# Kernel optimization log

Measured on AMD Instinct MI355X. Metric: run time of the kernel, lower is better.

Reference implementation:

```python
import jax, jax.numpy as jnp
import numpy as np

D_MODEL = 2048
N_HEADS = 32
N_KV = 8
HEAD_DIM = D_MODEL // N_HEADS  # 64
D_FF = 8192
ROPE_BASE = 10000.0
EPS = 1e-5
B, S = 2, 2048


def setup_inputs() -> dict:
    key = jax.random.key(0)
    ks = jax.random.split(key, 8)
    s = 0.02
    qkv_out = (N_HEADS + 2 * N_KV) * HEAD_DIM
    return {
        "x": jax.random.normal(ks[0], (B, S, D_MODEL), jnp.float32),
        "w_norm1": jnp.ones((D_MODEL,), jnp.float32),
        "w_qkv": jax.random.normal(ks[1], (D_MODEL, qkv_out), jnp.float32) * s,
        "w_out": jax.random.normal(ks[2], (D_MODEL, D_MODEL), jnp.float32) * s,
        "w_norm2": jnp.ones((D_MODEL,), jnp.float32),
        "w_gate": jax.random.normal(ks[3], (D_MODEL, D_FF), jnp.float32) * s,
        "w_up": jax.random.normal(ks[4], (D_MODEL, D_FF), jnp.float32) * s,
        "w_down": jax.random.normal(ks[5], (D_FF, D_MODEL), jnp.float32) * s,
    }


def _rmsnorm(x, w):
    var = jnp.mean(x * x, axis=-1, keepdims=True)
    return x * jax.lax.rsqrt(var + EPS) * w


def _rope(x, cos, sin):
    # x: [b, s, h, d]; cos/sin: [s, d/2]; non-interleaved (NeoX half split)
    half = x.shape[-1] // 2
    x1, x2 = x[..., :half], x[..., half:]
    c = cos[None, :, None, :]
    sn = sin[None, :, None, :]
    return jnp.concatenate([x1 * c - x2 * sn, x1 * sn + x2 * c], axis=-1)


def _forward(x, w_norm1, w_qkv, w_out, w_norm2, w_gate, w_up, w_down):
    b, s, d = x.shape
    # --- attention block ---
    h = _rmsnorm(x, w_norm1)
    qkv = h @ w_qkv  # [b, s, (H + 2*KV) * hd]
    q = qkv[..., : N_HEADS * HEAD_DIM].reshape(b, s, N_HEADS, HEAD_DIM)
    kv = qkv[..., N_HEADS * HEAD_DIM:].reshape(b, s, 2, N_KV, HEAD_DIM)
    k, v = kv[:, :, 0], kv[:, :, 1]

    inv_freq = 1.0 / (ROPE_BASE ** (jnp.arange(0, HEAD_DIM, 2, dtype=jnp.float32) / HEAD_DIM))
    t = jnp.arange(s, dtype=jnp.float32)
    freqs = t[:, None] * inv_freq[None, :]  # [s, hd/2]
    cos, sin = jnp.cos(freqs), jnp.sin(freqs)
    q = _rope(q, cos, sin)
    k = _rope(k, cos, sin)

    # GQA: repeat_interleave kv heads to match q heads
    g = N_HEADS // N_KV
    k = jnp.repeat(k, g, axis=2)  # [b, s, H, hd]
    v = jnp.repeat(v, g, axis=2)

    scale = 1.0 / np.sqrt(HEAD_DIM)
    scores = jnp.einsum("bqhd,bkhd->bhqk", q, k) * scale
    causal = jnp.tril(jnp.ones((s, s), bool))
    scores = jnp.where(causal[None, None], scores, jnp.finfo(scores.dtype).min)
    attn = jax.nn.softmax(scores, axis=-1)
    ctx = jnp.einsum("bhqk,bkhd->bqhd", attn, v).reshape(b, s, N_HEADS * HEAD_DIM)
    x = x + ctx @ w_out

    # --- MLP block (SwiGLU) ---
    h2 = _rmsnorm(x, w_norm2)
    mlp = (jax.nn.silu(h2 @ w_gate) * (h2 @ w_up)) @ w_down
    return x + mlp


def reference(x, w_norm1, w_qkv, w_out, w_norm2, w_gate, w_up, w_down):
    return _forward(x, w_norm1, w_qkv, w_out, w_norm2, w_gate, w_up, w_down)
```

## Files before the change

### kernel.cpp

```cpp
#include <hip/hip_runtime.h>
#include <stdint.h>

#define D_MODEL 2048
#define S_LEN   2048
#define NTOK    4096
#define QKV_N   3072
#define DFF     8192

typedef float  f32x4   __attribute__((ext_vector_type(4)));
typedef float  f32x16  __attribute__((ext_vector_type(16)));
typedef __bf16 bf16x8  __attribute__((ext_vector_type(8)));
typedef unsigned short u16;
typedef unsigned short u16x8 __attribute__((ext_vector_type(8)));

__device__ __forceinline__ float b2f(u16 u){ union{float f; uint32_t i;} v; v.i = ((uint32_t)u) << 16; return v.f; }
__device__ __forceinline__ u16 f2b(float f){
  union{float f; uint32_t i;} v; v.f = f;
  uint32_t r = v.i + 0x7FFFu + ((v.i >> 16) & 1u);
  return (u16)(r >> 16);
}

__device__ __forceinline__ void gload_lds16(const void* gsrc, void* ldst){
  __builtin_amdgcn_global_load_lds(
      (const __attribute__((address_space(1))) void*)gsrc,
      (__attribute__((address_space(3))) void*)ldst,
      16, 0, 0);
}

__global__ __launch_bounds__(256) void wconv_kernel(const float* __restrict__ W, u16* __restrict__ WT,
                                                    int Nfull, int Kt, int Nt, int k0g, int n0g)
{
  __shared__ float tile[64][65];
  const int nTn = Nt >> 6;
  const int tk = blockIdx.x / nTn, tn = blockIdx.x % nTn;
  const int k0 = tk << 6, n0 = tn << 6;
  const int t  = threadIdx.x;
  const int c4 = (t & 15) << 2;
  const int r  = t >> 4;
#pragma unroll
  for (int i = 0; i < 4; ++i) {
    float4 v = *reinterpret_cast<const float4*>(&W[(size_t)(k0g + k0 + r + i*16) * Nfull + n0g + n0 + c4]);
    tile[r + i*16][c4+0] = v.x; tile[r + i*16][c4+1] = v.y;
    tile[r + i*16][c4+2] = v.z; tile[r + i*16][c4+3] = v.w;
  }
  __syncthreads();
#pragma unroll
  for (int i = 0; i < 4; ++i) {
    int n = r + i*16;
    ushort4 ov;
    ov.x = f2b(tile[c4+0][n]); ov.y = f2b(tile[c4+1][n]);
    ov.z = f2b(tile[c4+2][n]); ov.w = f2b(tile[c4+3][n]);
    *reinterpret_cast<ushort4*>(&WT[(size_t)(n0 + n) * Kt + k0 + c4]) = ov;
  }
}

__global__ void sincos_kernel(float* __restrict__ ct, float* __restrict__ st)
{
  int idx = blockIdx.x * 256 + threadIdx.x;
  if (idx >= S_LEN * 32) return;
  int p = idx >> 5, i = idx & 31;
  double freq = pow(10000.0, -((double)(2*i)) / 64.0);
  double ang  = (double)p * freq;
  ct[idx] = (float)cos(ang);
  st[idx] = (float)sin(ang);
}

template<bool BF16IN>
__global__ __launch_bounds__(256) void rmsnorm_kernel(const void* __restrict__ xin, const float* __restrict__ w, u16* __restrict__ out)
{
  const int row = blockIdx.x;
  const int t = threadIdx.x;
  float v[8];
  if (BF16IN) {
    const u16* xr = ((const u16*)xin) + (size_t)row * D_MODEL;
    u16x8 a = *reinterpret_cast<const u16x8*>(&xr[t*8]);
#pragma unroll
    for (int j = 0; j < 8; ++j) v[j] = b2f(a[j]);
  } else {
    const float* xr = ((const float*)xin) + (size_t)row * D_MODEL;
    float4 a = *reinterpret_cast<const float4*>(&xr[t*8]);
    float4 c = *reinterpret_cast<const float4*>(&xr[t*8+4]);
    v[0]=a.x; v[1]=a.y; v[2]=a.z; v[3]=a.w; v[4]=c.x; v[5]=c.y; v[6]=c.z; v[7]=c.w;
  }
  float ss = 0.f;
#pragma unroll
  for (int j = 0; j < 8; ++j) ss += v[j]*v[j];
#pragma unroll
  for (int d = 1; d < 64; d <<= 1) ss += __shfl_xor(ss, d);
  __shared__ float red[4];
  if ((t & 63) == 0) red[t >> 6] = ss;
  __syncthreads();
  ss = red[0] + red[1] + red[2] + red[3];
  const float sc = rsqrtf(ss * (1.0f / (float)D_MODEL) + 1e-5f);
  float4 w0 = *reinterpret_cast<const float4*>(&w[t*8]);
  float4 w1 = *reinterpret_cast<const float4*>(&w[t*8+4]);
  u16x8 o;
  o[0]=f2b(v[0]*sc*w0.x); o[1]=f2b(v[1]*sc*w0.y); o[2]=f2b(v[2]*sc*w0.z); o[3]=f2b(v[3]*sc*w0.w);
  o[4]=f2b(v[4]*sc*w1.x); o[5]=f2b(v[5]*sc*w1.y); o[6]=f2b(v[6]*sc*w1.z); o[7]=f2b(v[7]*sc*w1.w);
  *reinterpret_cast<u16x8*>(&out[(size_t)row * D_MODEL + t*8]) = o;
}

template<int EPI>
__global__ __launch_bounds__(512, 2) void gemm8p_kernel(
    const u16* __restrict__ A, const u16* __restrict__ BT,
    int K, int lda, int ldb, int ldc, int n_off,
    float* Cf, u16* Cb,
    const float* __restrict__ resf, const u16* __restrict__ resb, const u16* other)
{
  __shared__ u16 lds[65536];
  const int tid = threadIdx.x;
  const int w = tid >> 6, lane = tid & 63;
  const int g = lane >> 4, lr = lane & 15;
  const int wm = w >> 2, wn = w & 3;
  const int bn = blockIdx.x, bm = blockIdx.y;
  const int NT = K >> 6;
  const int NI = NT >> 1;

  const int srow = tid >> 3;
  const int sg   = (tid & 7) ^ (srow & 7);
  const u16* Asrc = A  + (size_t)(bm * 256) * lda;
  const u16* Bsrc = BT + (size_t)(bn * 256) * ldb;

  const int agc0 = ((0 + g) ^ (lr & 7)) * 8;
  const int agc1 = ((4 + g) ^ (lr & 7)) * 8;

  f32x4 acc[8][4];
#pragma unroll
  for (int i = 0; i < 8; ++i)
#pragma unroll
    for (int j = 0; j < 4; ++j) acc[i][j] = (f32x4){0.f, 0.f, 0.f, 0.f};
  bf16x8 af[4][2], bf0[2][2], bf1[2][2];

#define STAGE_H(isB, h, b, T) do {                                           \
    int tc = ((T) < NT) ? (T) : (NT - 1);                                    \
    const u16* sb = (isB) ? Bsrc : Asrc;                                     \
    const int  sld = (isB) ? ldb : lda;                                      \
    const u16* s0 = sb + (size_t)((h)*128 + srow) * sld + tc*64 + sg*8;      \
    u16* dst = &lds[(b)*32768 + (isB)*16384 + (h)*8192 + tid*8];             \
    gload_lds16(s0, dst);                                                    \
    gload_lds16(s0 + (size_t)64 * sld, dst + 4096);                          \
  } while (0)

#define LOADA(mih, b) { _Pragma("unroll") for (int q = 0; q < 4; ++q) {      \
    const u16* rp = &lds[(b)*32768 + (wm*128 + (mih)*64 + q*16 + lr) * 64];  \
    af[q][0] = *(const bf16x8*)(rp + agc0);                                  \
    af[q][1] = *(const bf16x8*)(rp + agc1); } }

#define LOADB(dst, nih, b) { _Pragma("unroll") for (int nq = 0; nq < 2; ++nq) { \
    const u16* rp = &lds[(b)*32768 + 16384 + (wn*64 + (nih)*32 + nq*16 + lr) * 64]; \
    dst[nq][0] = *(const bf16x8*)(rp + agc0);                                \
    dst[nq][1] = *(const bf16x8*)(rp + agc1); } }

#define MM(mih, nih, BF) {                                                   \
    __builtin_amdgcn_s_setprio(1);                                           \
    _Pragma("unroll") for (int kk = 0; kk < 2; ++kk)                         \
      _Pragma("unroll") for (int q = 0; q < 4; ++q)                          \
        _Pragma("unroll") for (int nq = 0; nq < 2; ++nq)                     \
          acc[(mih)*4+q][(nih)*2+nq] = __builtin_amdgcn_mfma_f32_16x16x32_bf16( \
              af[q][kk], BF[nq][kk], acc[(mih)*4+q][(nih)*2+nq], 0, 0, 0);   \
    __builtin_amdgcn_s_setprio(0); }

#define SYNC_MID  __builtin_amdgcn_s_barrier();                              \
                  asm volatile("s_waitcnt lgkmcnt(0)" ::: "memory");         \
                  __builtin_amdgcn_sched_barrier(0);
#define PHEND     __builtin_amdgcn_s_barrier();
#define PHEND_VM  asm volatile("s_waitcnt vmcnt(4)" ::: "memory");           \
                  __builtin_amdgcn_s_barrier();

  STAGE_H(0, 0, 0, 0); STAGE_H(0, 1, 0, 0);
  STAGE_H(1, 0, 0, 0); STAGE_H(1, 1, 0, 0);
  STAGE_H(1, 0, 1, 1); STAGE_H(1, 1, 1, 1);
  asm volatile("s_waitcnt vmcnt(4)" ::: "memory");
  __builtin_amdgcn_s_barrier();

  for (int i = 0; i < NI; ++i) {
    const int t0 = 2 * i;
    LOADA(0, 0); LOADB(bf0, 0, 0);
    STAGE_H(0, 0, 1, t0 + 1);
    SYNC_MID; MM(0, 0, bf0); PHEND;
    LOADB(bf1, 1, 0);
    STAGE_H(0, 1, 1, t0 + 1);
    SYNC_MID; MM(0, 1, bf1); PHEND;
    LOADA(1, 0);
    STAGE_H(1, 0, 0, t0 + 2);
    SYNC_MID; MM(1, 1, bf1); PHEND;
    STAGE_H(1, 1, 0, t0 + 2);
    SYNC_MID; MM(1, 0, bf0); PHEND_VM;
    LOADA(0, 1); LOADB(bf0, 0, 1);
    STAGE_H(0, 0, 0, t0 + 2);
    SYNC_MID; MM(0, 0, bf0); PHEND;
    LOADB(bf1, 1, 1);
    STAGE_H(0, 1, 0, t0 + 2);
    SYNC_MID; MM(0, 1, bf1); PHEND;
    LOADA(1, 1);
    STAGE_H(1, 0, 1, t0 + 3);
    SYNC_MID; MM(1, 1, bf1); PHEND;
    STAGE_H(1, 1, 1, t0 + 3);
    SYNC_MID; MM(1, 0, bf0); PHEND_VM;
  }
#undef STAGE_H
#undef LOADA
#undef LOADB
#undef MM
#undef SYNC_MID
#undef PHEND
#undef PHEND_VM

#pragma unroll
  for (int mi = 0; mi < 8; ++mi) {
    const int rowOff = (mi >> 2) * 64 + (mi & 3) * 16;
#pragma unroll
    for (int ni = 0; ni < 4; ++ni) {
      const int colOff = (ni >> 1) * 32 + (ni & 1) * 16;
#pragma unroll
      for (int j = 0; j < 4; ++j) {
        int row = bm*256 + wm*128 + rowOff + g*4 + j;
        int col = n_off + bn*256 + wn*64 + colOff + lr;
        size_t idx = (size_t)row * ldc + col;
        float v = acc[mi][ni][j];
        if (EPI == 2)      Cb[idx] = f2b(v / (1.0f + __expf(-v)));
        else if (EPI == 3) Cb[idx] = f2b(v * b2f(other[idx]));
        else if (EPI == 4) Cb[idx] = f2b(v);
        else if (EPI == 5) Cf[idx] += v;
        else if (EPI == 6) Cb[idx] = f2b(v + resf[idx]);
        else if (EPI == 7) Cf[idx] = v + b2f(resb[idx]);
      }
    }
  }
}

__global__ __launch_bounds__(256) void rope_kernel(
    const u16* __restrict__ qkv, const float* __restrict__ ct, const float* __restrict__ st,
    u16* __restrict__ Q, u16* __restrict__ Kt, u16* __restrict__ VT)
{
  const int tok = blockIdx.x;
  const int b = tok >> 11, s = tok & (S_LEN - 1);
  const int w = threadIdx.x >> 6, lane = threadIdx.x & 63;
  const size_t base = (size_t)tok * QKV_N;
  for (int slot = w; slot < 48; slot += 4) {
    int col = (slot < 32) ? slot * 64 : (slot < 40 ? 2048 + (slot - 32) * 64 : 2560 + (slot - 40) * 64);
    float v = b2f(qkv[base + col + lane]);
    if (slot < 40) {
      int i = lane & 31;
      float c = ct[s * 32 + i], sn = st[s * 32 + i];
      float p = b2f(qkv[base + col + (lane ^ 32)]);
      v = (lane < 32) ? (v * c - p * sn) : (v * c + p * sn);
    }
    u16 ob = f2b(v);
    if (slot < 32)      Q [((size_t)(b * 32 + slot)      * S_LEN + s) * 64 + lane] = ob;
    else if (slot < 40) Kt[((size_t)(b * 8 + slot - 32)  * S_LEN + s) * 64 + lane] = ob;
    else                VT[((size_t)(b * 8 + slot - 40)  * 64 + lane) * S_LEN + s] = ob;
  }
}

#define ASCALE 0.1803368801111204f
__global__ __launch_bounds__(256, 3) void attn_kernel(
    const u16* __restrict__ Q, const u16* __restrict__ Kt,
    const u16* __restrict__ VT, u16* __restrict__ ctx)
{
  const int bh  = blockIdx.x;
  const int qb  = 15 - blockIdx.y;
  const int wid = threadIdx.x >> 6;
  const int lane = threadIdx.x & 63;
  const int b = bh >> 5, h = bh & 31;
  const int kvh = (b << 3) + (h >> 2);
  const int q0 = qb * 128 + wid * 32;
  const int cq = lane & 31;
  const int hi = lane >> 5;

  const u16* Qb = Q  + ((size_t)bh * S_LEN + q0) * 64;
  const u16* Kb = Kt + (size_t)kvh * S_LEN * 64;
  const u16* Vb = VT + (size_t)kvh * 64 * S_LEN;

  bf16x8 qf[4];
#pragma unroll
  for (int t = 0; t < 4; ++t)
    qf[t] = *reinterpret_cast<const bf16x8*>(&Qb[cq * 64 + t * 16 + hi * 8]);

  f32x16 o0 = {}, o1 = {};
  float m = -1e30f, l = 0.f;

  __shared__ float xch[4][32];

  const int nt = (q0 >> 5) + 1;
  for (int t = 0; t < nt; ++t) {
    const int k0 = t << 5;
    bf16x8 kf[4], vf[4];
#pragma unroll
    for (int tt = 0; tt < 4; ++tt)
      kf[tt] = *reinterpret_cast<const bf16x8*>(&Kb[(size_t)(k0 + cq) * 64 + tt * 16 + hi * 8]);
#pragma unroll
    for (int kh = 0; kh < 2; ++kh)
#pragma unroll
      for (int dh = 0; dh < 2; ++dh)
        vf[kh * 2 + dh] = *reinterpret_cast<const bf16x8*>(&Vb[(size_t)(dh * 32 + cq) * S_LEN + k0 + kh * 16 + hi * 8]);

    f32x16 sA = {}, sB = {};
    sA = __builtin_amdgcn_mfma_f32_32x32x16_bf16(kf[0], qf[0], sA, 0, 0, 0);
    sB = __builtin_amdgcn_mfma_f32_32x32x16_bf16(kf[1], qf[1], sB, 0, 0, 0);
    sA = __builtin_amdgcn_mfma_f32_32x32x16_bf16(kf[2], qf[2], sA, 0, 0, 0);
    sB = __builtin_amdgcn_mfma_f32_32x32x16_bf16(kf[3], qf[3], sB, 0, 0, 0);

    float p[16];
#pragma unroll
    for (int r = 0; r < 16; ++r) p[r] = (sA[r] + sB[r]) * ASCALE;
    if (t == nt - 1) {
#pragma unroll
      for (int r = 0; r < 16; ++r) {
        int kk = (r & 3) + 8 * (r >> 2) + 4 * hi;
        if (kk > cq) p[r] = -1e30f;
      }
    }
    float tmax = p[0];
#pragma unroll
    for (int r = 1; r < 16; ++r) tmax = fmaxf(tmax, p[r]);
    tmax = fmaxf(tmax, __shfl_xor(tmax, 32));

    if (!__all(tmax <= m + 8.0f)) {
      float mn = fmaxf(m, tmax);
      float corr = exp2f(m - mn);
      m = mn;
      l *= corr;
      if (hi == 0) xch[wid][cq] = corr;
      asm volatile("s_waitcnt lgkmcnt(0)" ::: "memory");
      __builtin_amdgcn_sched_barrier(0);
      float4 c0 = *reinterpret_cast<const float4*>(&xch[wid][4 * hi + 0]);
      float4 c1 = *reinterpret_cast<const float4*>(&xch[wid][4 * hi + 8]);
      float4 c2 = *reinterpret_cast<const float4*>(&xch[wid][4 * hi + 16]);
      float4 c3 = *reinterpret_cast<const float4*>(&xch[wid][4 * hi + 24]);
      float ca[16] = {c0.x,c0.y,c0.z,c0.w, c1.x,c1.y,c1.z,c1.w,
                      c2.x,c2.y,c2.z,c2.w, c3.x,c3.y,c3.z,c3.w};
#pragma unroll
      for (int r = 0; r < 16; ++r) { o0[r] *= ca[r]; o1[r] *= ca[r]; }
    }

    float ts = 0.f;
#pragma unroll
    for (int r = 0; r < 16; ++r) { p[r] = exp2f(p[r] - m); ts += p[r]; }
    ts += __shfl_xor(ts, 32);
    l += ts;

    uint32_t wds[8], pw[8];
#pragma unroll
    for (int j = 0; j < 8; ++j) {
      uint32_t wv;
      asm("v_cvt_pk_bf16_f32 %0, %1, %2" : "=v"(wv) : "v"(p[2*j]), "v"(p[2*j+1]));
      wds[j] = wv;
    }
#pragma unroll
    for (int j = 0; j < 8; ++j) pw[j] = __shfl_xor(wds[j], 32);
    union { uint32_t u[4]; bf16x8 v; } pa0, pa1;
    pa0.u[0] = hi ? pw[2]  : wds[0];
    pa0.u[1] = hi ? pw[3]  : wds[1];
    pa0.u[2] = hi ? wds[2] : pw[0];
    pa0.u[3] = hi ? wds[3] : pw[1];
    pa1.u[0] = hi ? pw[6]  : wds[4];
    pa1.u[1] = hi ? pw[7]  : wds[5];
    pa1.u[2] = hi ? wds[6] : pw[4];
    pa1.u[3] = hi ? wds[7] : pw[5];

    o0 = __builtin_amdgcn_mfma_f32_32x32x16_bf16(pa0.v, vf[0], o0, 0, 0, 0);
    o0 = __builtin_amdgcn_mfma_f32_32x32x16_bf16(pa1.v, vf[2], o0, 0, 0, 0);
    o1 = __builtin_amdgcn_mfma_f32_32x32x16_bf16(pa0.v, vf[1], o1, 0, 0, 0);
    o1 = __builtin_amdgcn_mfma_f32_32x32x16_bf16(pa1.v, vf[3], o1, 0, 0, 0);
  }

  float linv = 1.0f / l;
  if (hi == 0) xch[wid][cq] = linv;
  asm volatile("s_waitcnt lgkmcnt(0)" ::: "memory");
  __builtin_amdgcn_sched_barrier(0);
  float4 n0 = *reinterpret_cast<const float4*>(&xch[wid][4 * hi + 0]);
  float4 n1 = *reinterpret_cast<const float4*>(&xch[wid][4 * hi + 8]);
  float4 n2 = *reinterpret_cast<const float4*>(&xch[wid][4 * hi + 16]);
  float4 n3 = *reinterpret_cast<const float4*>(&xch[wid][4 * hi + 24]);
  float na[16] = {n0.x,n0.y,n0.z,n0.w, n1.x,n1.y,n1.z,n1.w,
                  n2.x,n2.y,n2.z,n2.w, n3.x,n3.y,n3.z,n3.w};
#pragma unroll
  for (int r = 0; r < 16; ++r) {
    int row = (r & 3) + 8 * (r >> 2) + 4 * hi;
    size_t base = (size_t)(b * S_LEN + q0 + row) * D_MODEL + h * 64;
    ctx[base + cq]      = f2b(o0[r] * na[r]);
    ctx[base + 32 + cq] = f2b(o1[r] * na[r]);
  }
}

extern "C" void kernel_launch(void* const* d_in, const int* in_sizes, int n_in,
                              void* d_out, int out_size, void* d_ws, size_t ws_size,
                              hipStream_t stream)
{
  const float* x     = (const float*)d_in[0];
  const float* wn1   = (const float*)d_in[1];
  const float* wqkv  = (const float*)d_in[2];
  const float* wout  = (const float*)d_in[3];
  const float* wn2   = (const float*)d_in[4];
  const float* wgate = (const float*)d_in[5];
  const float* wup   = (const float*)d_in[6];
  const float* wdown = (const float*)d_in[7];
  float* out = (float*)d_out;
  char* ws = (char*)d_ws;

  float* cosT = (float*)(ws + 0);
  float* sinT = (float*)(ws + 262144);
  u16*   wT   = (u16*)  (ws + 524288);
  u16*   hB   = (u16*)  (ws + 17301504);
  u16*   x1b  = (u16*)  (ws + 34078720);
  char*  S    = ws + 50855936;
  u16*   qkvB = (u16*)(S + 0);
  u16*   qB   = (u16*)(S + 25165824);
  u16*   kB   = (u16*)(S + 41943040);
  u16*   vtB  = (u16*)(S + 46137344);
  u16*   ctxB = (u16*)(S + 50331648);
  u16*   gsB  = (u16*)(S + 0);

  sincos_kernel<<<dim3(256), 256, 0, stream>>>(cosT, sinT);
  rmsnorm_kernel<false><<<dim3(NTOK), 256, 0, stream>>>(x, wn1, hB);

  wconv_kernel<<<dim3((2048/64)*(3072/64)), 256, 0, stream>>>(wqkv, wT, 3072, 2048, 3072, 0, 0);
  gemm8p_kernel<4><<<dim3(QKV_N/256, NTOK/256), 512, 0, stream>>>(hB, wT, 2048, 2048, 2048, 3072, 0, nullptr, qkvB, nullptr, nullptr, nullptr);
  rope_kernel<<<dim3(NTOK), 256, 0, stream>>>(qkvB, cosT, sinT, qB, kB, vtB);
  attn_kernel<<<dim3(64, 16), 256, 0, stream>>>(qB, kB, vtB, ctxB);

  wconv_kernel<<<dim3((2048/64)*(2048/64)), 256, 0, stream>>>(wout, wT, 2048, 2048, 2048, 0, 0);
  gemm8p_kernel<6><<<dim3(D_MODEL/256, NTOK/256), 512, 0, stream>>>(ctxB, wT, 2048, 2048, 2048, 2048, 0, nullptr, x1b, x, nullptr, nullptr);

  rmsnorm_kernel<true><<<dim3(NTOK), 256, 0, stream>>>(x1b, wn2, hB);

  for (int c = 0; c < 2; ++c) {
    wconv_kernel<<<dim3((2048/64)*(4096/64)), 256, 0, stream>>>(wgate, wT, 8192, 2048, 4096, 0, c*4096);
    gemm8p_kernel<2><<<dim3(4096/256, NTOK/256), 512, 0, stream>>>(hB, wT, 2048, 2048, 2048, 8192, c*4096, nullptr, gsB, nullptr, nullptr, nullptr);
  }
  for (int c = 0; c < 2; ++c) {
    wconv_kernel<<<dim3((2048/64)*(4096/64)), 256, 0, stream>>>(wup, wT, 8192, 2048, 4096, 0, c*4096);
    gemm8p_kernel<3><<<dim3(4096/256, NTOK/256), 512, 0, stream>>>(hB, wT, 2048, 2048, 2048, 8192, c*4096, nullptr, gsB, nullptr, nullptr, gsB);
  }
  wconv_kernel<<<dim3((4096/64)*(2048/64)), 256, 0, stream>>>(wdown, wT, 2048, 4096, 2048, 0, 0);
  gemm8p_kernel<7><<<dim3(D_MODEL/256, NTOK/256), 512, 0, stream>>>(gsB, wT, 4096, 8192, 4096, 2048, 0, out, nullptr, nullptr, x1b, nullptr);
  wconv_kernel<<<dim3((4096/64)*(2048/64)), 256, 0, stream>>>(wdown, wT, 2048, 4096, 2048, 4096, 0);
  gemm8p_kernel<5><<<dim3(D_MODEL/256, NTOK/256), 512, 0, stream>>>(gsB + 4096, wT, 4096, 8192, 4096, 2048, 0, out, nullptr, nullptr, nullptr, nullptr);
}
```

Before: 900.3 us.

## Add 128-row GEMM for small-N projections and split-K causal attention for late query blocks

Adds a 128x256-tile GEMM variant and uses it for the QKV, output and down projections. The smaller M tile doubles the block count on these narrow-N GEMMs so more of the GPU's compute units are busy. Attention now splits the key range of the eight longest causal query blocks across two workgroups, writing partial outputs with their max and sum statistics. A new combine kernel merges the two partials, which balances per-block work in exchange for an extra launch and more global traffic.

```diff
diff --git a/kernel.cpp b/kernel.cpp
--- a/kernel.cpp
+++ b/kernel.cpp
@@ -98,6 +98,18 @@
   o[0]=f2b(v[0]*sc*w0.x); o[1]=f2b(v[1]*sc*w0.y); o[2]=f2b(v[2]*sc*w0.z); o[3]=f2b(v[3]*sc*w0.w);
   o[4]=f2b(v[4]*sc*w1.x); o[5]=f2b(v[5]*sc*w1.y); o[6]=f2b(v[6]*sc*w1.z); o[7]=f2b(v[7]*sc*w1.w);
   *reinterpret_cast<u16x8*>(&out[(size_t)row * D_MODEL + t*8]) = o;
+}
+
+template<int EPI>
+__device__ __forceinline__ void epi_store(size_t idx, float v, float* Cf, u16* Cb,
+                                          const float* resf, const u16* resb, const u16* other)
+{
+  if (EPI == 2)      Cb[idx] = f2b(v / (1.0f + __expf(-v)));
+  else if (EPI == 3) Cb[idx] = f2b(v * b2f(other[idx]));
+  else if (EPI == 4) Cb[idx] = f2b(v);
+  else if (EPI == 5) Cf[idx] += v;
+  else if (EPI == 6) Cb[idx] = f2b(v + resf[idx]);
+  else if (EPI == 7) Cf[idx] = v + b2f(resb[idx]);
 }
 
 template<int EPI>
@@ -202,28 +214,141 @@
 #undef LOADA
 #undef LOADB
 #undef MM
+
+#pragma unroll
+  for (int mi = 0; mi < 8; ++mi) {
+    const int rowOff = (mi >> 2) * 64 + (mi & 3) * 16;
+#pragma unroll
+    for (int ni = 0; ni < 4; ++ni) {
+      const int colOff = (ni >> 1) * 32 + (ni & 1) * 16;
+#pragma unroll
+      for (int j = 0; j < 4; ++j) {
+        int row = bm*256 + wm*128 + rowOff + g*4 + j;
+        int col = n_off + bn*256 + wn*64 + colOff + lr;
+        epi_store<EPI>((size_t)row * ldc + col, acc[mi][ni][j], Cf, Cb, resf, resb, other);
+      }
+    }
+  }
+}
+
+template<int EPI>
+__global__ __launch_bounds__(512) void gemm128_kernel(
+    const u16* __restrict__ A, const u16* __restrict__ BT,
+    int K, int lda, int ldb, int ldc, int n_off,
+    float* Cf, u16* Cb,
+    const float* __restrict__ resf, const u16* __restrict__ resb, const u16* other)
+{
+  __shared__ u16 lds[49152];
+  const int tid = threadIdx.x;
+  const int w = tid >> 6, lane = tid & 63;
+  const int g = lane >> 4, lr = lane & 15;
+  const int wm = w >> 2, wn = w & 3;
+  const int bn = blockIdx.x, bm = blockIdx.y;
+  const int NT = K >> 6;
+  const int NI = NT >> 1;
+
+  const int srow = tid >> 3;
+  const int sg   = (tid & 7) ^ (srow & 7);
+  const u16* Asrc = A  + (size_t)(bm * 128) * lda;
+  const u16* Bsrc = BT + (size_t)(bn * 256) * ldb;
+
+  const int agc0 = ((0 + g) ^ (lr & 7)) * 8;
+  const int agc1 = ((4 + g) ^ (lr & 7)) * 8;
+
+  f32x4 acc[4][4];
+#pragma unroll
+  for (int i = 0; i < 4; ++i)
+#pragma unroll
+    for (int j = 0; j < 4; ++j) acc[i][j] = (f32x4){0.f, 0.f, 0.f, 0.f};
+  bf16x8 af[2][2], bf0[2][2], bf1[2][2];
+
+#define STAGE_A(b, T) do {                                                   \
+    int tc = ((T) < NT) ? (T) : (NT - 1);                                    \
+    const u16* s0 = Asrc + (size_t)srow * lda + tc*64 + sg*8;                \
+    u16* dst = &lds[(b)*24576 + tid*8];                                      \
+    gload_lds16(s0, dst);                                                    \
+    gload_lds16(s0 + (size_t)64 * lda, dst + 4096);                          \
+  } while (0)
+
+#define STAGE_BH(h, b, T) do {                                               \
+    int tc = ((T) < NT) ? (T) : (NT - 1);                                    \
+    const u16* s0 = Bsrc + (size_t)((h)*128 + srow) * ldb + tc*64 + sg*8;    \
+    u16* dst = &lds[(b)*24576 + 8192 + (h)*8192 + tid*8];                    \
+    gload_lds16(s0, dst);                                                    \
+    gload_lds16(s0 + (size_t)64 * ldb, dst + 4096);                         \
+  } while (0)
+
+#define LOADA(mih, b) { _Pragma("unroll") for (int q = 0; q < 2; ++q) {      \
+    const u16* rp = &lds[(b)*24576 + (wm*64 + (mih)*32 + q*16 + lr) * 64];   \
+    af[q][0] = *(const bf16x8*)(rp + agc0);                                  \
+    af[q][1] = *(const bf16x8*)(rp + agc1); } }
+
+#define LOADB(dst, nih, b) { _Pragma("unroll") for (int nq = 0; nq < 2; ++nq) { \
+    const u16* rp = &lds[(b)*24576 + 8192 + (wn*64 + (nih)*32 + nq*16 + lr) * 64]; \
+    dst[nq][0] = *(const bf16x8*)(rp + agc0);                                \
+    dst[nq][1] = *(const bf16x8*)(rp + agc1); } }
+
+#define MM(mih, nih, BF) {                                                   \
+    __builtin_amdgcn_s_setprio(1);                                           \
+    _Pragma("unroll") for (int kk = 0; kk < 2; ++kk)                         \
+      _Pragma("unroll") for (int q = 0; q < 2; ++q)                          \
+        _Pragma("unroll") for (int nq = 0; nq < 2; ++nq)                     \
+          acc[(mih)*2+q][(nih)*2+nq] = __builtin_amdgcn_mfma_f32_16x16x32_bf16( \
+              af[q][kk], BF[nq][kk], acc[(mih)*2+q][(nih)*2+nq], 0, 0, 0);   \
+    __builtin_amdgcn_s_setprio(0); }
+
+  STAGE_A(0, 0); STAGE_BH(0, 0, 0); STAGE_BH(1, 0, 0);
+  STAGE_BH(0, 1, 1); STAGE_BH(1, 1, 1);
+  asm volatile("s_waitcnt vmcnt(4)" ::: "memory");
+  __builtin_amdgcn_s_barrier();
+
+  for (int i = 0; i < NI; ++i) {
+    const int t0 = 2 * i;
+    LOADA(0, 0); LOADB(bf0, 0, 0);
+    STAGE_A(1, t0 + 1);
+    SYNC_MID; MM(0, 0, bf0); PHEND;
+    LOADB(bf1, 1, 0);
+    STAGE_BH(0, 0, t0 + 2);
+    SYNC_MID; MM(0, 1, bf1); PHEND;
+    LOADA(1, 0);
+    STAGE_BH(1, 0, t0 + 2);
+    SYNC_MID; MM(1, 1, bf1); PHEND;
+    STAGE_A(0, t0 + 2);
+    SYNC_MID; MM(1, 0, bf0);
+    asm volatile("s_waitcnt vmcnt(6)" ::: "memory");
+    __builtin_amdgcn_s_barrier();
+    LOADA(0, 1); LOADB(bf0, 0, 1);
+    SYNC_MID; MM(0, 0, bf0); PHEND;
+    LOADB(bf1, 1, 1);
+    STAGE_BH(0, 1, t0 + 3);
+    SYNC_MID; MM(0, 1, bf1); PHEND;
+    LOADA(1, 1);
+    STAGE_BH(1, 1, t0 + 3);
+    SYNC_MID; MM(1, 1, bf1); PHEND;
+    SYNC_MID; MM(1, 0, bf0);
+    asm volatile("s_waitcnt vmcnt(4)" ::: "memory");
+    __builtin_amdgcn_s_barrier();
+  }
+#undef STAGE_A
+#undef STAGE_BH
+#undef LOADA
+#undef LOADB
+#undef MM
 #undef SYNC_MID
 #undef PHEND
 #undef PHEND_VM
 
 #pragma unroll
-  for (int mi = 0; mi < 8; ++mi) {
-    const int rowOff = (mi >> 2) * 64 + (mi & 3) * 16;
+  for (int mi = 0; mi < 4; ++mi) {
+    const int rowOff = (mi >> 1) * 32 + (mi & 1) * 16;
 #pragma unroll
     for (int ni = 0; ni < 4; ++ni) {
       const int colOff = (ni >> 1) * 32 + (ni & 1) * 16;
 #pragma unroll
       for (int j = 0; j < 4; ++j) {
-        int row = bm*256 + wm*128 + rowOff + g*4 + j;
+        int row = bm*128 + wm*64 + rowOff + g*4 + j;
         int col = n_off + bn*256 + wn*64 + colOff + lr;
-        size_t idx = (size_t)row * ldc + col;
-        float v = acc[mi][ni][j];
-        if (EPI == 2)      Cb[idx] = f2b(v / (1.0f + __expf(-v)));
-        else if (EPI == 3) Cb[idx] = f2b(v * b2f(other[idx]));
-        else if (EPI == 4) Cb[idx] = f2b(v);
-        else if (EPI == 5) Cf[idx] += v;
-        else if (EPI == 6) Cb[idx] = f2b(v + resf[idx]);
-        else if (EPI == 7) Cf[idx] = v + b2f(resb[idx]);
+        epi_store<EPI>((size_t)row * ldc + col, acc[mi][ni][j], Cf, Cb, resf, resb, other);
       }
     }
   }
@@ -256,10 +381,14 @@
 #define ASCALE 0.1803368801111204f
 __global__ __launch_bounds__(256, 3) void attn_kernel(
     const u16* __restrict__ Q, const u16* __restrict__ Kt,
-    const u16* __restrict__ VT, u16* __restrict__ ctx)
+    const u16* __restrict__ VT, u16* __restrict__ ctx,
+    u16* __restrict__ po, float2* __restrict__ pml)
 {
   const int bh  = blockIdx.x;
-  const int qb  = 15 - blockIdx.y;
+  const int y   = blockIdx.y;
+  int qb, split;
+  if (y < 16) { qb = 15 - (y >> 1); split = y & 1; }
+  else        { qb = 23 - y;        split = -1;    }
   const int wid = threadIdx.x >> 6;
   const int lane = threadIdx.x & 63;
   const int b = bh >> 5, h = bh & 31;
@@ -282,8 +411,11 @@
 
   __shared__ float xch[4][32];
 
-  const int nt = (q0 >> 5) + 1;
-  for (int t = 0; t < nt; ++t) {
+  const int nt = qb * 4 + wid + 1;
+  const int ts = (split == 1) ? (nt >> 1) : 0;
+  const int te = (split == 0) ? (nt >> 1) : nt;
+
+  for (int t = ts; t < te; ++t) {
     const int k0 = t << 5;
     bf16x8 kf[4], vf[4];
 #pragma unroll
@@ -334,11 +466,11 @@
       for (int r = 0; r < 16; ++r) { o0[r] *= ca[r]; o1[r] *= ca[r]; }
     }
 
-    float ts = 0.f;
-#pragma unroll
-    for (int r = 0; r < 16; ++r) { p[r] = exp2f(p[r] - m); ts += p[r]; }
-    ts += __shfl_xor(ts, 32);
-    l += ts;
+    float tsum = 0.f;
+#pragma unroll
+    for (int r = 0; r < 16; ++r) { p[r] = exp2f(p[r] - m); tsum += p[r]; }
+    tsum += __shfl_xor(tsum, 32);
+    l += tsum;
 
     uint32_t wds[8], pw[8];
 #pragma unroll
@@ -365,22 +497,56 @@
     o1 = __builtin_amdgcn_mfma_f32_32x32x16_bf16(pa1.v, vf[3], o1, 0, 0, 0);
   }
 
-  float linv = 1.0f / l;
-  if (hi == 0) xch[wid][cq] = linv;
-  asm volatile("s_waitcnt lgkmcnt(0)" ::: "memory");
-  __builtin_amdgcn_sched_barrier(0);
-  float4 n0 = *reinterpret_cast<const float4*>(&xch[wid][4 * hi + 0]);
-  float4 n1 = *reinterpret_cast<const float4*>(&xch[wid][4 * hi + 8]);
-  float4 n2 = *reinterpret_cast<const float4*>(&xch[wid][4 * hi + 16]);
-  float4 n3 = *reinterpret_cast<const float4*>(&xch[wid][4 * hi + 24]);
-  float na[16] = {n0.x,n0.y,n0.z,n0.w, n1.x,n1.y,n1.z,n1.w,
-                  n2.x,n2.y,n2.z,n2.w, n3.x,n3.y,n3.z,n3.w};
-#pragma unroll
-  for (int r = 0; r < 16; ++r) {
-    int row = (r & 3) + 8 * (r >> 2) + 4 * hi;
-    size_t base = (size_t)(b * S_LEN + q0 + row) * D_MODEL + h * 64;
-    ctx[base + cq]      = f2b(o0[r] * na[r]);
-    ctx[base + 32 + cq] = f2b(o1[r] * na[r]);
+  if (split < 0) {
+    float linv = 1.0f / l;
+    if (hi == 0) xch[wid][cq] = linv;
+    asm volatile("s_waitcnt lgkmcnt(0)" ::: "memory");
+    __builtin_amdgcn_sched_barrier(0);
+    float4 n0 = *reinterpret_cast<const float4*>(&xch[wid][4 * hi + 0]);
+    float4 n1 = *reinterpret_cast<const float4*>(&xch[wid][4 * hi + 8]);
+    float4 n2 = *reinterpret_cast<const float4*>(&xch[wid][4 * hi + 16]);
+    float4 n3 = *reinterpret_cast<const float4*>(&xch[wid][4 * hi + 24]);
+    float na[16] = {n0.x,n0.y,n0.z,n0.w, n1.x,n1.y,n1.z,n1.w,
+                    n2.x,n2.y,n2.z,n2.w, n3.x,n3.y,n3.z,n3.w};
+#pragma unroll
+    for (int r = 0; r < 16; ++r) {
+      int row = (r & 3) + 8 * (r >> 2) + 4 * hi;
+      size_t base = (size_t)(b * S_LEN + q0 + row) * D_MODEL + h * 64;
+      ctx[base + cq]      = f2b(o0[r] * na[r]);
+      ctx[base + 32 + cq] = f2b(o1[r] * na[r]);
+    }
+  } else {
+    const int qr0 = q0 - 1024;
+    if (hi == 0) {
+      float2 v; v.x = m; v.y = l;
+      pml[((size_t)(split * 64 + bh)) * 1024 + qr0 + cq] = v;
+    }
+#pragma unroll
+    for (int r = 0; r < 16; ++r) {
+      int row = (r & 3) + 8 * (r >> 2) + 4 * hi;
+      size_t base = (((size_t)(split * 64 + bh)) * 1024 + qr0 + row) * 64;
+      po[base + cq]      = f2b(o0[r]);
+      po[base + 32 + cq] = f2b(o1[r]);
+    }
+  }
+}
+
+__global__ __launch_bounds__(256) void attn_combine(
+    const u16* __restrict__ po, const float2* __restrict__ pml, u16* __restrict__ ctx)
+{
+  const int bh = blockIdx.x;
+  const int b = bh >> 5, h = bh & 31;
+  const int d = threadIdx.x & 63;
+  for (int rr = threadIdx.x >> 6; rr < 64; rr += 4) {
+    const int qr = blockIdx.y * 64 + rr;
+    float2 ml1 = pml[(size_t)bh * 1024 + qr];
+    float2 ml2 = pml[(size_t)(64 + bh) * 1024 + qr];
+    float mm = fmaxf(ml1.x, ml2.x);
+    float w1 = exp2f(ml1.x - mm), w2 = exp2f(ml2.x - mm);
+    float denom = ml1.y * w1 + ml2.y * w2;
+    float v1 = b2f(po[((size_t)bh * 1024 + qr) * 64 + d]);
+    float v2 = b2f(po[((size_t)(64 + bh) * 1024 + qr) * 64 + d]);
+    ctx[((size_t)(b * S_LEN) + 1024 + qr) * D_MODEL + h * 64 + d] = f2b((v1 * w1 + v2 * w2) / denom);
   }
 }
 
@@ -406,6 +572,8 @@
   u16*   x1b  = (u16*)  (ws + 34078720);
   char*  S    = ws + 50855936;
   u16*   qkvB = (u16*)(S + 0);
+  u16*   poB  = (u16*)(S + 0);
+  float2* pmlB= (float2*)(S + 16777216);
   u16*   qB   = (u16*)(S + 25165824);
   u16*   kB   = (u16*)(S + 41943040);
   u16*   vtB  = (u16*)(S + 46137344);
@@ -416,12 +584,13 @@
   rmsnorm_kernel<false><<<dim3(NTOK), 256, 0, stream>>>(x, wn1, hB);
 
   wconv_kernel<<<dim3((2048/64)*(3072/64)), 256, 0, stream>>>(wqkv, wT, 3072, 2048, 3072, 0, 0);
-  gemm8p_kernel<4><<<dim3(QKV_N/256, NTOK/256), 512, 0, stream>>>(hB, wT, 2048, 2048, 2048, 3072, 0, nullptr, qkvB, nullptr, nullptr, nullptr);
+  gemm128_kernel<4><<<dim3(QKV_N/256, NTOK/128), 512, 0, stream>>>(hB, wT, 2048, 2048, 2048, 3072, 0, nullptr, qkvB, nullptr, nullptr, nullptr);
   rope_kernel<<<dim3(NTOK), 256, 0, stream>>>(qkvB, cosT, sinT, qB, kB, vtB);
-  attn_kernel<<<dim3(64, 16), 256, 0, stream>>>(qB, kB, vtB, ctxB);
+  attn_kernel<<<dim3(64, 24), 256, 0, stream>>>(qB, kB, vtB, ctxB, poB, pmlB);
+  attn_combine<<<dim3(64, 16), 256, 0, stream>>>(poB, pmlB, ctxB);
 
   wconv_kernel<<<dim3((2048/64)*(2048/64)), 256, 0, stream>>>(wout, wT, 2048, 2048, 2048, 0, 0);
-  gemm8p_kernel<6><<<dim3(D_MODEL/256, NTOK/256), 512, 0, stream>>>(ctxB, wT, 2048, 2048, 2048, 2048, 0, nullptr, x1b, x, nullptr, nullptr);
+  gemm128_kernel<6><<<dim3(D_MODEL/256, NTOK/128), 512, 0, stream>>>(ctxB, wT, 2048, 2048, 2048, 2048, 0, nullptr, x1b, x, nullptr, nullptr);
 
   rmsnorm_kernel<true><<<dim3(NTOK), 256, 0, stream>>>(x1b, wn2, hB);
 
@@ -434,7 +603,7 @@
     gemm8p_kernel<3><<<dim3(4096/256, NTOK/256), 512, 0, stream>>>(hB, wT, 2048, 2048, 2048, 8192, c*4096, nullptr, gsB, nullptr, nullptr, gsB);
   }
   wconv_kernel<<<dim3((4096/64)*(2048/64)), 256, 0, stream>>>(wdown, wT, 2048, 4096, 2048, 0, 0);
-  gemm8p_kernel<7><<<dim3(D_MODEL/256, NTOK/256), 512, 0, stream>>>(gsB, wT, 4096, 8192, 4096, 2048, 0, out, nullptr, nullptr, x1b, nullptr);
+  gemm128_kernel<7><<<dim3(D_MODEL/256, NTOK/128), 512, 0, stream>>>(gsB, wT, 4096, 8192, 4096, 2048, 0, out, nullptr, nullptr, x1b, nullptr);
   wconv_kernel<<<dim3((4096/64)*(2048/64)), 256, 0, stream>>>(wdown, wT, 2048, 4096, 2048, 4096, 0);
-  gemm8p_kernel<5><<<dim3(D_MODEL/256, NTOK/256), 512, 0, stream>>>(gsB + 4096, wT, 4096, 8192, 4096, 2048, 0, out, nullptr, nullptr, nullptr, nullptr);
-}
+  gemm128_kernel<5><<<dim3(D_MODEL/256, NTOK/128), 512, 0, stream>>>(gsB + 4096, wT, 4096, 8192, 4096, 2048, 0, out, nullptr, nullptr, nullptr, nullptr);
+}
```

New measurement: 826.4 us. 1.09x faster.
